# Kernel tuning notes

Measured on AMD Instinct MI355X. Metric: run time of the kernel, lower is better.

Reference implementation:

```python
import jax, jax.numpy as jnp
import numpy as np

B, C, H, W = 32, 17, 256, 256


def setup_inputs() -> dict:
    key = jax.random.key(0)
    k1, k2 = jax.random.split(key)
    inp = jax.random.normal(k1, (B, C, H, W), dtype=jnp.float32)
    tgt = jax.random.normal(k2, (B, C, H, W), dtype=jnp.float32)
    masks = jnp.zeros((B, C, H, W), dtype=bool)  # unused by forward
    hull = jnp.zeros((B, 1, H, W), dtype=bool)   # unused by forward
    return {"input": inp, "target": tgt, "masks": masks, "hull": hull}


def reference(input, target, masks, hull):
    # m1: per-(batch, channel) mask of positive target pixels
    m1 = target > 0.0                                  # [B,C,H,W] bool
    # m2: per-batch OR over channels, broadcast back to every channel.
    # (replaces the original O(B*C) Python double loop)
    m2 = jnp.any(m1, axis=1, keepdims=True)            # [B,1,H,W] bool
    diff = jnp.abs(input - target)                     # [B,C,H,W]
    f32 = jnp.float32
    # masked means without data-dependent shapes: sum(mask*diff)/sum(mask)
    mean1 = jnp.sum(jnp.where(m1, diff, f32(0))) / jnp.sum(m1).astype(f32)
    cnt2 = jnp.sum(m2).astype(f32) * f32(diff.shape[1])  # broadcast over C channels
    mean2 = jnp.sum(jnp.where(m2, diff, f32(0))) / cnt2
    return (mean1 + mean2) / f32(2)
```

## Files before the change

kernel.cpp:

```cpp
#include <hip/hip_runtime.h>


typedef unsigned long long u64;
typedef unsigned int u32;

#define N_CH       17
#define QPP        16384
#define N_PLANES   (32 * N_CH)
#define N_QUADS    (N_PLANES * QPP)
#define GRID1      2048
#define ITERS      17
#define MASK_WORDS 32768
#define SLOT_OFF   (MASK_WORDS * 8)

struct Slot { float s1, s2; u32 c1, c2; };


__global__ __launch_bounds__(256) void mask_zero(u64* __restrict__ mask) {
    mask[blockIdx.x * 256 + threadIdx.x] = 0ULL;
}

__global__ __launch_bounds__(256) void mask_build(const float* __restrict__ tgt,
                                                  u64* __restrict__ mask) {
    const float4* __restrict__ t4 = (const float4*)tgt;
    int f = blockIdx.x * 256 + threadIdx.x;
    const int lane = threadIdx.x & 63;
    #pragma unroll 1
    for (int it = 0; it < ITERS; ++it, f += GRID1 * 256) {
        float4 t = t4[f];
        u64 b0 = __ballot(t.x > 0.f);
        u64 b1 = __ballot(t.y > 0.f);
        u64 b2 = __ballot(t.z > 0.f);
        u64 b3 = __ballot(t.w > 0.f);
        int plane = f >> 14;
        int b = plane / N_CH;
        int grp = b * 256 + ((f & (QPP - 1)) >> 6);
        if (lane < 4) {
            u64 w = (lane == 0) ? b0 : (lane == 1) ? b1 : (lane == 2) ? b2 : b3;
            if (w) atomicOr(&mask[(size_t)grp * 4 + lane], w);
        }
    }
}

__global__ __launch_bounds__(256) void heat_main(const float* __restrict__ inp,
                                                 const float* __restrict__ tgt,
                                                 const u64* __restrict__ mask,
                                                 Slot* __restrict__ slots) {
    const float4* __restrict__ t4 = (const float4*)tgt;
    const float4* __restrict__ x4 = (const float4*)inp;

    float s1 = 0.f, s2 = 0.f;
    u32 c1 = 0u, c2 = 0u;
    int f = blockIdx.x * 256 + threadIdx.x;
    const int lane = threadIdx.x & 63;

    #pragma unroll 1
    for (int it = 0; it < ITERS; ++it, f += GRID1 * 256) {
        float4 t = t4[f];
        float4 x = x4[f];

        int plane = f >> 14;
        int b = plane / N_CH;
        int grp = b * 256 + ((f & (QPP - 1)) >> 6);
        u32 g = __builtin_amdgcn_readfirstlane((u32)grp);
        const u64* __restrict__ mw = mask + (size_t)g * 4;
        u64 w0 = mw[0], w1 = mw[1], w2 = mw[2], w3 = mw[3];

        float d0 = fabsf(x.x - t.x);
        float d1 = fabsf(x.y - t.y);
        float d2 = fabsf(x.z - t.z);
        float d3 = fabsf(x.w - t.w);

        bool p0 = t.x > 0.f, p1 = t.y > 0.f, p2 = t.z > 0.f, p3 = t.w > 0.f;
        s1 += p0 ? d0 : 0.f;  c1 += p0 ? 1u : 0u;
        s1 += p1 ? d1 : 0.f;  c1 += p1 ? 1u : 0u;
        s1 += p2 ? d2 : 0.f;  c1 += p2 ? 1u : 0u;
        s1 += p3 ? d3 : 0.f;  c1 += p3 ? 1u : 0u;

        u32 m0 = (u32)((w0 >> lane) & 1ULL);
        u32 m1 = (u32)((w1 >> lane) & 1ULL);
        u32 m2 = (u32)((w2 >> lane) & 1ULL);
        u32 m3 = (u32)((w3 >> lane) & 1ULL);
        s2 += m0 ? d0 : 0.f;  c2 += m0;
        s2 += m1 ? d1 : 0.f;  c2 += m1;
        s2 += m2 ? d2 : 0.f;  c2 += m2;
        s2 += m3 ? d3 : 0.f;  c2 += m3;
    }

    #pragma unroll
    for (int off = 32; off > 0; off >>= 1) {
        s1 += __shfl_down(s1, off);
        s2 += __shfl_down(s2, off);
        c1 += __shfl_down(c1, off);
        c2 += __shfl_down(c2, off);
    }
    __shared__ float ls1[4], ls2[4];
    __shared__ u32 lc1[4], lc2[4];
    const int wave = threadIdx.x >> 6;
    if (lane == 0) { ls1[wave] = s1; ls2[wave] = s2; lc1[wave] = c1; lc2[wave] = c2; }
    __syncthreads();
    if (threadIdx.x == 0) {
        Slot sl;
        sl.s1 = ls1[0] + ls1[1] + ls1[2] + ls1[3];
        sl.s2 = ls2[0] + ls2[1] + ls2[2] + ls2[3];
        sl.c1 = lc1[0] + lc1[1] + lc1[2] + lc1[3];
        sl.c2 = lc2[0] + lc2[1] + lc2[2] + lc2[3];
        slots[blockIdx.x] = sl;
    }
}

__global__ __launch_bounds__(256) void final_reduce(const Slot* __restrict__ slots,
                                                    float* __restrict__ out) {
    float s1 = 0.f, s2 = 0.f;
    u32 c1 = 0u, c2 = 0u;
    for (int i = threadIdx.x; i < GRID1; i += 256) {
        Slot sl = slots[i];
        s1 += sl.s1; s2 += sl.s2; c1 += sl.c1; c2 += sl.c2;
    }
    #pragma unroll
    for (int off = 32; off > 0; off >>= 1) {
        s1 += __shfl_down(s1, off);
        s2 += __shfl_down(s2, off);
        c1 += __shfl_down(c1, off);
        c2 += __shfl_down(c2, off);
    }
    __shared__ float ls1[4], ls2[4];
    __shared__ u32 lc1[4], lc2[4];
    const int wave = threadIdx.x >> 6;
    const int lane = threadIdx.x & 63;
    if (lane == 0) { ls1[wave] = s1; ls2[wave] = s2; lc1[wave] = c1; lc2[wave] = c2; }
    __syncthreads();
    if (threadIdx.x == 0) {
        float S1 = ls1[0] + ls1[1] + ls1[2] + ls1[3];
        float S2 = ls2[0] + ls2[1] + ls2[2] + ls2[3];
        float C1 = (float)(lc1[0] + lc1[1] + lc1[2] + lc1[3]);
        float C2 = (float)(lc2[0] + lc2[1] + lc2[2] + lc2[3]);
        float mean1 = S1 / C1;
        float mean2 = S2 / C2;
        out[0] = 0.5f * (mean1 + mean2);
    }
}

extern "C" void kernel_launch(void* const* d_in, const int* in_sizes, int n_in,
                              void* d_out, int out_size, void* d_ws, size_t ws_size,
                              hipStream_t stream) {
    const float* inp = (const float*)d_in[0];
    const float* tgt = (const float*)d_in[1];
    float* out = (float*)d_out;
    u64* mask = (u64*)d_ws;
    Slot* slots = (Slot*)((char*)d_ws + SLOT_OFF);

    mask_zero<<<128, 256, 0, stream>>>(mask);
    mask_build<<<GRID1, 256, 0, stream>>>(tgt, mask);
    heat_main<<<GRID1, 256, 0, stream>>>(inp, tgt, mask, slots);
    final_reduce<<<1, 256, 0, stream>>>(slots, out);
}
```

Baseline: 350.9 us.

## Fuse mask build into main sweep and subtract unmasked pixels in fixup

```diff
diff --git a/kernel.cpp b/kernel.cpp
--- a/kernel.cpp
+++ b/kernel.cpp
@@ -6,136 +6,157 @@
 
 #define N_CH       17
 #define QPP        16384
-#define N_PLANES   (32 * N_CH)
-#define N_QUADS    (N_PLANES * QPP)
+#define N_QUADS    (32 * N_CH * QPP)
 #define GRID1      2048
+#define STRIDE     (GRID1 * 256)
 #define ITERS      17
-#define MASK_WORDS 32768
+#define N_GROUPS   8192
+#define MASK_WORDS (N_GROUPS * 4)
 #define SLOT_OFF   (MASK_WORDS * 8)
+#define N_PIX      2097152u
 
-struct Slot { float s1, s2; u32 c1, c2; };
-
+struct Slot { float s1, sall; u32 c1, pad; };
 
 __global__ __launch_bounds__(256) void mask_zero(u64* __restrict__ mask) {
     mask[blockIdx.x * 256 + threadIdx.x] = 0ULL;
 }
 
-__global__ __launch_bounds__(256) void mask_build(const float* __restrict__ tgt,
-                                                  u64* __restrict__ mask) {
+__global__ __launch_bounds__(256, 8) void heat_sweep(
+    const float* __restrict__ inp, const float* __restrict__ tgt,
+    u64* __restrict__ mask, Slot* __restrict__ slots) {
+
     const float4* __restrict__ t4 = (const float4*)tgt;
+    const float4* __restrict__ x4 = (const float4*)inp;
+
+    const int lane = threadIdx.x & 63;
     int f = blockIdx.x * 256 + threadIdx.x;
-    const int lane = threadIdx.x & 63;
+
+    float s1 = 0.f, sall = 0.f;
+    u32 c1 = 0u;
+
+    float4 t = t4[f];
+    float4 x = x4[f];
+
     #pragma unroll 1
-    for (int it = 0; it < ITERS; ++it, f += GRID1 * 256) {
-        float4 t = t4[f];
-        u64 b0 = __ballot(t.x > 0.f);
-        u64 b1 = __ballot(t.y > 0.f);
-        u64 b2 = __ballot(t.z > 0.f);
-        u64 b3 = __ballot(t.w > 0.f);
-        int plane = f >> 14;
+    for (int it = 0; it < ITERS; ++it) {
+        float4 tc = t, xc = x;
+        const int fc = f;
+        if (it + 1 < ITERS) {
+            f += STRIDE;
+            t = t4[f];
+            x = x4[f];
+        }
+
+        float d0 = fabsf(xc.x - tc.x);
+        float d1 = fabsf(xc.y - tc.y);
+        float d2 = fabsf(xc.z - tc.z);
+        float d3 = fabsf(xc.w - tc.w);
+        sall += (d0 + d1) + (d2 + d3);
+
+        bool p0 = tc.x > 0.f, p1 = tc.y > 0.f, p2 = tc.z > 0.f, p3 = tc.w > 0.f;
+        s1 += p0 ? d0 : 0.f;  c1 += p0 ? 1u : 0u;
+        s1 += p1 ? d1 : 0.f;  c1 += p1 ? 1u : 0u;
+        s1 += p2 ? d2 : 0.f;  c1 += p2 ? 1u : 0u;
+        s1 += p3 ? d3 : 0.f;  c1 += p3 ? 1u : 0u;
+
+        u64 b0 = __ballot(p0);
+        u64 b1 = __ballot(p1);
+        u64 b2 = __ballot(p2);
+        u64 b3 = __ballot(p3);
+
+        int plane = fc >> 14;
         int b = plane / N_CH;
-        int grp = b * 256 + ((f & (QPP - 1)) >> 6);
+        int grp = (b << 8) + ((fc & (QPP - 1)) >> 6);
         if (lane < 4) {
             u64 w = (lane == 0) ? b0 : (lane == 1) ? b1 : (lane == 2) ? b2 : b3;
             if (w) atomicOr(&mask[(size_t)grp * 4 + lane], w);
         }
     }
-}
-
-__global__ __launch_bounds__(256) void heat_main(const float* __restrict__ inp,
-                                                 const float* __restrict__ tgt,
-                                                 const u64* __restrict__ mask,
-                                                 Slot* __restrict__ slots) {
-    const float4* __restrict__ t4 = (const float4*)tgt;
-    const float4* __restrict__ x4 = (const float4*)inp;
-
-    float s1 = 0.f, s2 = 0.f;
-    u32 c1 = 0u, c2 = 0u;
-    int f = blockIdx.x * 256 + threadIdx.x;
-    const int lane = threadIdx.x & 63;
-
-    #pragma unroll 1
-    for (int it = 0; it < ITERS; ++it, f += GRID1 * 256) {
-        float4 t = t4[f];
-        float4 x = x4[f];
-
-        int plane = f >> 14;
-        int b = plane / N_CH;
-        int grp = b * 256 + ((f & (QPP - 1)) >> 6);
-        u32 g = __builtin_amdgcn_readfirstlane((u32)grp);
-        const u64* __restrict__ mw = mask + (size_t)g * 4;
-        u64 w0 = mw[0], w1 = mw[1], w2 = mw[2], w3 = mw[3];
-
-        float d0 = fabsf(x.x - t.x);
-        float d1 = fabsf(x.y - t.y);
-        float d2 = fabsf(x.z - t.z);
-        float d3 = fabsf(x.w - t.w);
-
-        bool p0 = t.x > 0.f, p1 = t.y > 0.f, p2 = t.z > 0.f, p3 = t.w > 0.f;
-        s1 += p0 ? d0 : 0.f;  c1 += p0 ? 1u : 0u;
-        s1 += p1 ? d1 : 0.f;  c1 += p1 ? 1u : 0u;
-        s1 += p2 ? d2 : 0.f;  c1 += p2 ? 1u : 0u;
-        s1 += p3 ? d3 : 0.f;  c1 += p3 ? 1u : 0u;
-
-        u32 m0 = (u32)((w0 >> lane) & 1ULL);
-        u32 m1 = (u32)((w1 >> lane) & 1ULL);
-        u32 m2 = (u32)((w2 >> lane) & 1ULL);
-        u32 m3 = (u32)((w3 >> lane) & 1ULL);
-        s2 += m0 ? d0 : 0.f;  c2 += m0;
-        s2 += m1 ? d1 : 0.f;  c2 += m1;
-        s2 += m2 ? d2 : 0.f;  c2 += m2;
-        s2 += m3 ? d3 : 0.f;  c2 += m3;
-    }
 
     #pragma unroll
     for (int off = 32; off > 0; off >>= 1) {
-        s1 += __shfl_down(s1, off);
-        s2 += __shfl_down(s2, off);
-        c1 += __shfl_down(c1, off);
-        c2 += __shfl_down(c2, off);
+        s1   += __shfl_down(s1, off);
+        sall += __shfl_down(sall, off);
+        c1   += __shfl_down(c1, off);
     }
-    __shared__ float ls1[4], ls2[4];
-    __shared__ u32 lc1[4], lc2[4];
+    __shared__ float ls1[4], lsa[4];
+    __shared__ u32 lc1[4];
     const int wave = threadIdx.x >> 6;
-    if (lane == 0) { ls1[wave] = s1; ls2[wave] = s2; lc1[wave] = c1; lc2[wave] = c2; }
+    if (lane == 0) { ls1[wave] = s1; lsa[wave] = sall; lc1[wave] = c1; }
     __syncthreads();
     if (threadIdx.x == 0) {
         Slot sl;
-        sl.s1 = ls1[0] + ls1[1] + ls1[2] + ls1[3];
-        sl.s2 = ls2[0] + ls2[1] + ls2[2] + ls2[3];
-        sl.c1 = lc1[0] + lc1[1] + lc1[2] + lc1[3];
-        sl.c2 = lc2[0] + lc2[1] + lc2[2] + lc2[3];
+        sl.s1   = ls1[0] + ls1[1] + ls1[2] + ls1[3];
+        sl.sall = lsa[0] + lsa[1] + lsa[2] + lsa[3];
+        sl.c1   = lc1[0] + lc1[1] + lc1[2] + lc1[3];
+        sl.pad  = 0u;
         slots[blockIdx.x] = sl;
     }
 }
 
-__global__ __launch_bounds__(256) void final_reduce(const Slot* __restrict__ slots,
-                                                    float* __restrict__ out) {
-    float s1 = 0.f, s2 = 0.f;
-    u32 c1 = 0u, c2 = 0u;
-    for (int i = threadIdx.x; i < GRID1; i += 256) {
+__global__ __launch_bounds__(256) void fixup(
+    const float* __restrict__ inp, const float* __restrict__ tgt,
+    const u64* __restrict__ mask, const Slot* __restrict__ slots,
+    float* __restrict__ out) {
+
+    const int tid = threadIdx.x;
+    float s1 = 0.f, sall = 0.f;
+    u32 c1 = 0u;
+    for (int i = tid; i < GRID1; i += 256) {
         Slot sl = slots[i];
-        s1 += sl.s1; s2 += sl.s2; c1 += sl.c1; c2 += sl.c2;
+        s1 += sl.s1; sall += sl.sall; c1 += sl.c1;
     }
+
+    float sub = 0.f;
+    u32 nz = 0u;
+    for (int wi = tid; wi < MASK_WORDS; wi += 256) {
+        u64 z = ~mask[wi];
+        if (z) {
+            const int g = wi >> 2;
+            const int j = wi & 3;
+            const int b = g >> 8;
+            const int baseq = (g & 255) << 6;
+            nz += (u32)__popcll(z);
+            while (z) {
+                int l = __builtin_ctzll(z);
+                z &= z - 1;
+                int pix = ((baseq + l) << 2) + j;
+                size_t base = ((size_t)b * N_CH) << 16;
+                #pragma unroll
+                for (int c = 0; c < N_CH; ++c) {
+                    size_t off = base + ((size_t)c << 16) + (size_t)pix;
+                    sub += fabsf(inp[off] - tgt[off]);
+                }
+            }
+        }
+    }
+
+    const int lane = tid & 63;
+    const int wave = tid >> 6;
     #pragma unroll
     for (int off = 32; off > 0; off >>= 1) {
-        s1 += __shfl_down(s1, off);
-        s2 += __shfl_down(s2, off);
-        c1 += __shfl_down(c1, off);
-        c2 += __shfl_down(c2, off);
+        s1   += __shfl_down(s1, off);
+        sall += __shfl_down(sall, off);
+        sub  += __shfl_down(sub, off);
+        c1   += __shfl_down(c1, off);
+        nz   += __shfl_down(nz, off);
     }
-    __shared__ float ls1[4], ls2[4];
-    __shared__ u32 lc1[4], lc2[4];
-    const int wave = threadIdx.x >> 6;
-    const int lane = threadIdx.x & 63;
-    if (lane == 0) { ls1[wave] = s1; ls2[wave] = s2; lc1[wave] = c1; lc2[wave] = c2; }
+    __shared__ float ls1[4], lsa[4], lsb[4];
+    __shared__ u32 lc1[4], lnz[4];
+    if (lane == 0) {
+        ls1[wave] = s1; lsa[wave] = sall; lsb[wave] = sub;
+        lc1[wave] = c1; lnz[wave] = nz;
+    }
     __syncthreads();
-    if (threadIdx.x == 0) {
-        float S1 = ls1[0] + ls1[1] + ls1[2] + ls1[3];
-        float S2 = ls2[0] + ls2[1] + ls2[2] + ls2[3];
-        float C1 = (float)(lc1[0] + lc1[1] + lc1[2] + lc1[3]);
-        float C2 = (float)(lc2[0] + lc2[1] + lc2[2] + lc2[3]);
-        float mean1 = S1 / C1;
+    if (tid == 0) {
+        float S1   = ls1[0] + ls1[1] + ls1[2] + ls1[3];
+        float SALL = lsa[0] + lsa[1] + lsa[2] + lsa[3];
+        float SUB  = lsb[0] + lsb[1] + lsb[2] + lsb[3];
+        u32   C1   = lc1[0] + lc1[1] + lc1[2] + lc1[3];
+        u32   NZ   = lnz[0] + lnz[1] + lnz[2] + lnz[3];
+        float S2 = SALL - SUB;
+        float C2 = (float)(N_PIX - NZ) * (float)N_CH;
+        float mean1 = S1 / (float)C1;
         float mean2 = S2 / C2;
         out[0] = 0.5f * (mean1 + mean2);
     }
@@ -151,7 +172,6 @@
     Slot* slots = (Slot*)((char*)d_ws + SLOT_OFF);
 
     mask_zero<<<128, 256, 0, stream>>>(mask);
-    mask_build<<<GRID1, 256, 0, stream>>>(tgt, mask);
-    heat_main<<<GRID1, 256, 0, stream>>>(inp, tgt, mask, slots);
-    final_reduce<<<1, 256, 0, stream>>>(slots, out);
+    heat_sweep<<<GRID1, 256, 0, stream>>>(inp, tgt, mask, slots);
+    fixup<<<1, 256, 0, stream>>>(inp, tgt, mask, slots, out);
 }
```

Result: slower. 428.4 us (+22.1%).
